# Performance work log

Measured on AMD Instinct MI355X. Metric: run time of the kernel, lower is better.

The kernel has to match this reference:

```python
import jax, jax.numpy as jnp
import numpy as np

KDIM = 16

def setup_inputs() -> dict:
    key = jax.random.key(0)
    k1, k2, k3, k4 = jax.random.split(key, 4)
    bs, k, din, dout, T = 512, 8, 1024, 1024, 8
    x = jax.random.normal(k1, (bs, k, din), dtype=jnp.float32)
    # template weights: list of (din, dout) params -> stacked (T, din, dout)
    w = 0.01 * jax.random.normal(k2, (T, din, dout), dtype=jnp.float32)
    # gll_read: GroupLinearLayer(din, kdim, 1) -> (1, din, kdim)
    w_read = 0.01 * jax.random.normal(k3, (1, din, KDIM), dtype=jnp.float32)
    # gll_write: GroupLinearLayer(dout, kdim, T) -> (T, dout, kdim)
    w_write = 0.01 * jax.random.normal(k4, (T, dout, KDIM), dtype=jnp.float32)
    return {"x": x, "w": w, "w_read": w_read, "w_write": w_write}

def reference(x, w, w_read, w_write):
    bs, k, din = x.shape
    dout = w.shape[-1]
    xf = x.reshape(bs * k, din)                       # (N, din)
    x_read = xf @ w_read[0]                           # (N, kdim)  query per token
    x_next = jnp.einsum('nd,tde->nte', xf, w)         # (N, T, dout) all template outputs
    x_write = jnp.einsum('nte,tek->ntk', x_next, w_write)  # (N, T, kdim) keys
    logits = jnp.einsum('nk,ntk->nt', x_read, x_write)     # (N, T)
    att = jax.nn.softmax(logits, axis=-1)                  # softmax over templates
    out = jnp.einsum('nt,nte->ne', att, x_next)            # weighted combine (mean over size-1 dim is identity)
    return out.reshape(bs, k, dout)
```

## Files before the change

kernel.cpp:

```cpp
#include <hip/hip_runtime.h>
#include <stdint.h>

typedef unsigned short u16;
typedef __attribute__((ext_vector_type(8))) short bf16x8;
typedef __attribute__((ext_vector_type(4))) float f32x4;
typedef __attribute__((ext_vector_type(4))) unsigned short u16x4;

#define AS1 __attribute__((address_space(1)))
#define AS3 __attribute__((address_space(3)))

static __device__ __forceinline__ u16 f2bf(float f) {
  union { float f; uint32_t u; } c; c.f = f;
  return (u16)((c.u + 0x7FFFu + ((c.u >> 16) & 1u)) >> 16);
}

__global__ __launch_bounds__(256) void k_prep(const float* __restrict__ x,
                                              u16* __restrict__ abf,
                                              const float* __restrict__ w,
                                              u16* __restrict__ bt,
                                              const float* __restrict__ ww,
                                              float* __restrict__ w2s) {
  __shared__ char smem[16896];
  const int bid = blockIdx.x;
  const int tid = threadIdx.x;

  if (bid < 256) {
    float (*wwT)[264] = (float(*)[264])smem;
    const int lane = tid & 63, wv = tid >> 6;
    const int t = (bid >> 3) & 7;
    const int d0 = (bid & 7) * 128 + wv * 32;
    const int ez4 = bid >> 6;
    const int ez = ez4 * 256;
    const int fr = lane & 15, koff = (lane >> 4) * 8;
    const float* wp = w + ((size_t)t << 20);
    const float* wwp = ww + (t << 14);
    for (int it = 0; it < 16; ++it) {
      int idx = it * 256 + tid;
      wwT[idx & 15][idx >> 4] = wwp[(size_t)(ez + (idx >> 4)) * 16 + (idx & 15)];
    }
    __syncthreads();
    f32x4 acc[2] = {};
    for (int kk = 0; kk < 256; kk += 32) {
      const int eL = kk + koff;
      float4 b0 = *(const float4*)&wwT[fr][eL];
      float4 b1 = *(const float4*)&wwT[fr][eL + 4];
      bf16x8 b;
      ((u16*)&b)[0] = f2bf(b0.x); ((u16*)&b)[1] = f2bf(b0.y);
      ((u16*)&b)[2] = f2bf(b0.z); ((u16*)&b)[3] = f2bf(b0.w);
      ((u16*)&b)[4] = f2bf(b1.x); ((u16*)&b)[5] = f2bf(b1.y);
      ((u16*)&b)[6] = f2bf(b1.z); ((u16*)&b)[7] = f2bf(b1.w);
#pragma unroll
      for (int m = 0; m < 2; ++m) {
        const float* ap = wp + (size_t)(d0 + m * 16 + fr) * 1024 + ez + eL;
        float4 a0 = *(const float4*)ap;
        float4 a1 = *(const float4*)(ap + 4);
        bf16x8 a;
        ((u16*)&a)[0] = f2bf(a0.x); ((u16*)&a)[1] = f2bf(a0.y);
        ((u16*)&a)[2] = f2bf(a0.z); ((u16*)&a)[3] = f2bf(a0.w);
        ((u16*)&a)[4] = f2bf(a1.x); ((u16*)&a)[5] = f2bf(a1.y);
        ((u16*)&a)[6] = f2bf(a1.z); ((u16*)&a)[7] = f2bf(a1.w);
        acc[m] = __builtin_amdgcn_mfma_f32_16x16x32_bf16(a, b, acc[m], 0, 0, 0);
      }
    }
    float* slot = w2s + ((size_t)ez4 << 17);
#pragma unroll
    for (int m = 0; m < 2; ++m)
#pragma unroll
      for (int i = 0; i < 4; ++i) {
        int d = d0 + m * 16 + ((lane >> 4) << 2) + i;
        slot[(((size_t)t << 10) + d) * 16 + fr] = acc[m][i];
      }
  } else if (bid < 4352) {
    int i = (bid - 256) * 256 + tid;
    float4 v = reinterpret_cast<const float4*>(x)[i];
    u16x4 o = { f2bf(v.x), f2bf(v.y), f2bf(v.z), f2bf(v.w) };
    reinterpret_cast<u16x4*>(abf)[i] = o;
  } else {
    u16 (*tile)[65] = (u16(*)[65])smem;
    const int tb = bid - 4352;
    const int t = tb >> 8, rem = tb & 255;
    const int e0 = (rem & 15) * 64, d0 = (rem >> 4) * 64;
    const int tx = tid & 63, ty = tid >> 6;
    const float* wp = w + ((size_t)t << 20);
    u16* bp = bt + ((size_t)t << 20);
    for (int rr = 0; rr < 16; ++rr) {
      int r = rr * 4 + ty;
      tile[r][tx] = f2bf(wp[(size_t)(d0 + r) * 1024 + (e0 + tx)]);
    }
    __syncthreads();
    for (int rr = 0; rr < 16; ++rr) {
      int r = rr * 4 + ty;
      bp[(size_t)(e0 + r) * 1024 + (d0 + tx)] = tile[tx][r];
    }
  }
}

__global__ __launch_bounds__(256) void k_bt2(const float* __restrict__ wread,
                                             const float* __restrict__ w2s,
                                             u16* __restrict__ bt2) {
  int i = blockIdx.x * 256 + threadIdx.x;
  int r = i >> 10, d = i & 1023;
  float v;
  if (r < 16) v = wread[d * 16 + r];
  else {
    int t = (r - 16) >> 4, k = (r - 16) & 15;
    size_t off = (((size_t)t << 10) + d) * 16 + k;
    v = w2s[off] + w2s[(1ull << 17) + off] + w2s[(2ull << 17) + off]
      + w2s[(3ull << 17) + off];
  }
  bt2[i] = f2bf(v);
}

__global__ __launch_bounds__(256) void k_p(const u16* __restrict__ abf,
                                           const u16* __restrict__ bt2,
                                           float* __restrict__ Ps) {
  const int tid = threadIdx.x, lane = tid & 63, wv = tid >> 6;
  const int row0 = blockIdx.x * 64 + wv * 16;
  const int k0 = blockIdx.y * 256;
  const int fr = lane & 15, koff = (lane >> 4) * 8;
  f32x4 acc[9] = {};
  for (int kk = 0; kk < 256; kk += 32) {
    bf16x8 a = *(const bf16x8*)&abf[(size_t)(row0 + fr) * 1024 + k0 + kk + koff];
#pragma unroll
    for (int n = 0; n < 9; ++n) {
      bf16x8 b = *(const bf16x8*)&bt2[(size_t)(n * 16 + fr) * 1024 + k0 + kk + koff];
      acc[n] = __builtin_amdgcn_mfma_f32_16x16x32_bf16(a, b, acc[n], 0, 0, 0);
    }
  }
  float* slot = Ps + (size_t)blockIdx.y * 589824;
  const int rbase = row0 + ((lane >> 4) << 2);
#pragma unroll
  for (int n = 0; n < 9; ++n)
#pragma unroll
    for (int i = 0; i < 4; ++i)
      slot[(size_t)(rbase + i) * 144 + n * 16 + fr] = acc[n][i];
}

__global__ __launch_bounds__(256) void k_soft(const float* __restrict__ Ps,
                                              float* __restrict__ att) {
  __shared__ float lg[32][8];
  const int rl = threadIdx.x >> 3, tt = threadIdx.x & 7;
  const int r = blockIdx.x * 32 + rl;
  const float* p = Ps + (size_t)r * 144;
  f32x4 x0 = {}, x1 = {}, x2 = {}, x3 = {};
  f32x4 y0 = {}, y1 = {}, y2 = {}, y3 = {};
#pragma unroll
  for (int z = 0; z < 4; ++z) {
    const float* pz = p + (size_t)z * 589824;
    x0 += *(const f32x4*)(pz);      x1 += *(const f32x4*)(pz + 4);
    x2 += *(const f32x4*)(pz + 8);  x3 += *(const f32x4*)(pz + 12);
    const float* qz = pz + 16 + tt * 16;
    y0 += *(const f32x4*)(qz);      y1 += *(const f32x4*)(qz + 4);
    y2 += *(const f32x4*)(qz + 8);  y3 += *(const f32x4*)(qz + 12);
  }
  float acc = x0[0]*y0[0] + x0[1]*y0[1] + x0[2]*y0[2] + x0[3]*y0[3]
            + x1[0]*y1[0] + x1[1]*y1[1] + x1[2]*y1[2] + x1[3]*y1[3]
            + x2[0]*y2[0] + x2[1]*y2[1] + x2[2]*y2[2] + x2[3]*y2[3]
            + x3[0]*y3[0] + x3[1]*y3[1] + x3[2]*y3[2] + x3[3]*y3[3];
  lg[rl][tt] = acc;
  __syncthreads();
  float m = lg[rl][0];
#pragma unroll
  for (int j = 1; j < 8; ++j) m = fmaxf(m, lg[rl][j]);
  float s = 0.f;
#pragma unroll
  for (int j = 0; j < 8; ++j) s += __expf(lg[rl][j] - m);
  att[(size_t)r * 8 + tt] = __expf(lg[rl][tt] - m) / s;
}

#define BAR()   asm volatile("s_barrier" ::: "memory")
#define LGKM0() asm volatile("s_waitcnt lgkmcnt(0)" ::: "memory")
#define VM6()   asm volatile("s_waitcnt vmcnt(6)" ::: "memory")
#define VM0()   asm volatile("s_waitcnt vmcnt(0)" ::: "memory")

template <int MODE>
__global__ __launch_bounds__(512, 2) void k_gemm256(const u16* __restrict__ abf,
                                                    const u16* __restrict__ bt,
                                                    const float* __restrict__ att,
                                                    float* __restrict__ out,
                                                    char* __restrict__ part) {
  __shared__ char lds[133120];
  float* lAtt = (float*)(lds + 131072);

  const int tid = threadIdx.x;
  const int lane = tid & 63;
  const int wv = tid >> 6;
  const int wr = wv >> 2, wc = wv & 3;

  int id = (blockIdx.z * gridDim.y + blockIdx.y) * gridDim.x + blockIdx.x;
  const int xcd = id & 7, pos = id >> 3;
  const int bz = xcd >> 1;
  const int by = (xcd & 1) * 8 + (pos & 7);
  const int bx = pos >> 3;
  const int bm = by * 256, bn = bx * 256, t0 = bz * 2;

  { int r = tid >> 1, c = tid & 1;
    lAtt[r * 2 + c] = att[(size_t)(bm + r) * 8 + t0 + c]; }

  const int l7 = lane & 7, lq = lane >> 4, l15 = lane & 15;
  const int srow = lane >> 3;
  const int scg = l7 ^ srow;
  const char* Abase = (const char*)abf;
  const char* Bbase = (const char*)bt;
  const size_t aSt0 = (size_t)(bm + wv * 16 + srow) * 2048 + scg * 16;
  const size_t bSt0 = (size_t)(bn + wv * 16 + srow) * 2048 + scg * 16;
  const int sDst = wv * 2048;
  const int aRd = (wr * 64 + l15) * 128;
  const int bRd = 32768 + (wc * 32 + l15) * 128;
  const int g0 = ((lq) ^ l7) * 16;
  const int g1 = ((4 + lq) ^ l7) * 16;

#define STAGE_A(bufo, h, tile) do {                                         \
    const char* s_ = Abase + aSt0 + (size_t)(h) * 262144 + ((tile) & 15) * 128; \
    __builtin_amdgcn_global_load_lds((const AS1 void*)s_,                   \
        (AS3 void*)(lds + (bufo) + (h) * 16384 + sDst), 16, 0, 0);          \
    __builtin_amdgcn_global_load_lds((const AS1 void*)(s_ + 16384),         \
        (AS3 void*)(lds + (bufo) + (h) * 16384 + sDst + 1024), 16, 0, 0);   \
  } while (0)
#define STAGE_B(bufo, g, tile) do {                                         \
    const char* s_ = Bbase + (size_t)(t0 + ((tile) >> 4)) * 2097152         \
                   + bSt0 + (size_t)(g) * 262144 + ((tile) & 15) * 128;     \
    __builtin_amdgcn_global_load_lds((const AS1 void*)s_,                   \
        (AS3 void*)(lds + (bufo) + 32768 + (g) * 16384 + sDst), 16, 0, 0);  \
    __builtin_amdgcn_global_load_lds((const AS1 void*)(s_ + 16384),         \
        (AS3 void*)(lds + (bufo) + 32768 + (g) * 16384 + sDst + 1024), 16, 0, 0); \
  } while (0)
#define LDA(bufo, h) do {                                                   \
    const char* p_ = lds + (bufo) + (h) * 16384 + aRd;                      \
    _Pragma("unroll") for (int mm = 0; mm < 4; ++mm) {                      \
      a[mm][0] = *(const bf16x8*)(p_ + mm * 2048 + g0);                     \
      a[mm][1] = *(const bf16x8*)(p_ + mm * 2048 + g1); }                   \
  } while (0)
#define LDB(bufo, g, br) do {                                               \
    const char* p_ = lds + (bufo) + (g) * 16384 + bRd;                      \
    _Pragma("unroll") for (int nn = 0; nn < 2; ++nn) {                      \
      br[nn][0] = *(const bf16x8*)(p_ + nn * 2048 + g0);                    \
      br[nn][1] = *(const bf16x8*)(p_ + nn * 2048 + g1); }                  \
  } while (0)
#define MFQ(h, g, br) do {                                                  \
    __builtin_amdgcn_s_setprio(1);                                          \
    _Pragma("unroll") for (int mm = 0; mm < 4; ++mm)                        \
    _Pragma("unroll") for (int nn = 0; nn < 2; ++nn) {                      \
      acc[(h)*4+mm][(g)*2+nn] = __builtin_amdgcn_mfma_f32_16x16x32_bf16(    \
          a[mm][0], br[nn][0], acc[(h)*4+mm][(g)*2+nn], 0, 0, 0);           \
      acc[(h)*4+mm][(g)*2+nn] = __builtin_amdgcn_mfma_f32_16x16x32_bf16(    \
          a[mm][1], br[nn][1], acc[(h)*4+mm][(g)*2+nn], 0, 0, 0); }         \
    __builtin_amdgcn_s_setprio(0);                                          \
  } while (0)

  f32x4 acc[8][4] = {};
  bf16x8 a[4][2], b0[2][2], b1[2][2];

  STAGE_A(0, 0, 0); STAGE_B(0, 0, 0); STAGE_B(0, 1, 0); STAGE_A(0, 1, 0);
  STAGE_A(65536, 0, 1); STAGE_B(65536, 0, 1); STAGE_B(65536, 1, 1);
  VM6(); BAR();

  for (int i = 0; i < 15; ++i) {
    if (i == 8) {
#pragma unroll
      for (int m = 0; m < 8; ++m) {
        const int h_ = m >> 2, mm_ = m & 3;
#pragma unroll
        for (int ii = 0; ii < 4; ++ii) {
          const int r_ = h_ * 128 + wr * 64 + mm_ * 16 + lq * 4 + ii;
          const float sc = lAtt[r_ * 2] / lAtt[r_ * 2 + 1];
#pragma unroll
          for (int n = 0; n < 4; ++n) acc[m][n][ii] *= sc;
        }
      }
    }
    const int j1 = 2 * i + 1, j2 = 2 * i + 2, j3 = 2 * i + 3;
    LDA(0, 0); LDB(0, 0, b0); STAGE_A(65536, 1, j1);
    BAR(); LGKM0(); MFQ(0, 0, b0); BAR();
    LDB(0, 1, b1); STAGE_A(0, 0, j2);
    BAR(); LGKM0(); MFQ(0, 1, b1); BAR();
    LDA(0, 1); STAGE_B(0, 0, j2);
    BAR(); LGKM0(); MFQ(1, 1, b1); BAR();
    STAGE_B(0, 1, j2);
    BAR(); MFQ(1, 0, b0); VM6(); BAR();
    LDA(65536, 0); LDB(65536, 0, b0); STAGE_A(0, 1, j2);
    BAR(); LGKM0(); MFQ(0, 0, b0); BAR();
    LDB(65536, 1, b1); STAGE_A(65536, 0, j3);
    BAR(); LGKM0(); MFQ(0, 1, b1); BAR();
    LDA(65536, 1); STAGE_B(65536, 0, j3);
    BAR(); LGKM0(); MFQ(1, 1, b1); BAR();
    STAGE_B(65536, 1, j3);
    BAR(); MFQ(1, 0, b0); VM6(); BAR();
  }
  LDA(0, 0); LDB(0, 0, b0); STAGE_A(65536, 1, 31);
  BAR(); LGKM0(); MFQ(0, 0, b0); BAR();
  LDB(0, 1, b1);
  BAR(); LGKM0(); MFQ(0, 1, b1); BAR();
  LDA(0, 1);
  BAR(); LGKM0(); MFQ(1, 1, b1); BAR();
  BAR(); MFQ(1, 0, b0); VM0(); BAR();
  LDA(65536, 0); LDB(65536, 0, b0);
  BAR(); LGKM0(); MFQ(0, 0, b0); BAR();
  LDB(65536, 1, b1);
  BAR(); LGKM0(); MFQ(0, 1, b1); BAR();
  LDA(65536, 1);
  BAR(); LGKM0(); MFQ(1, 1, b1); BAR();
  BAR(); MFQ(1, 0, b0); BAR();

#pragma unroll
  for (int m = 0; m < 8; ++m) {
    const int h_ = m >> 2, mm_ = m & 3;
#pragma unroll
    for (int ii = 0; ii < 4; ++ii) {
      const int rl = h_ * 128 + wr * 64 + mm_ * 16 + lq * 4 + ii;
      const float sc = lAtt[rl * 2 + 1];
      const int row = bm + rl;
#pragma unroll
      for (int n = 0; n < 4; ++n) {
        const int g_ = n >> 1, nn_ = n & 1;
        const int col = bn + g_ * 128 + wc * 32 + nn_ * 16 + l15;
        const float v = acc[m][n][ii] * sc;
        if (MODE == 0) {
          unsafeAtomicAdd(&out[(size_t)row * 1024 + col], v);
        } else {
          ((u16*)part)[((size_t)bz << 22) + (size_t)row * 1024 + col] = f2bf(v);
        }
      }
    }
  }
#undef STAGE_A
#undef STAGE_B
#undef LDA
#undef LDB
#undef MFQ
}

__global__ __launch_bounds__(256) void k_reduce(const char* __restrict__ part,
                                                float* __restrict__ out) {
  const size_t i = ((size_t)blockIdx.x * 256 + threadIdx.x) * 4;
  const u16* p = (const u16*)part;
  f32x4 s = {};
#pragma unroll
  for (int z = 0; z < 4; ++z) {
    u16x4 v = *(const u16x4*)(p + ((size_t)z << 22) + i);
#pragma unroll
    for (int j = 0; j < 4; ++j) {
      union { uint32_t u; float f; } c; c.u = ((uint32_t)v[j]) << 16;
      s[j] += c.f;
    }
  }
  *(f32x4*)(out + i) = s;
}

extern "C" void kernel_launch(void* const* d_in, const int* in_sizes, int n_in,
                              void* d_out, int out_size, void* d_ws, size_t ws_size,
                              hipStream_t stream) {
  (void)in_sizes; (void)n_in;
  const float* x      = (const float*)d_in[0];
  const float* w      = (const float*)d_in[1];
  const float* wread  = (const float*)d_in[2];
  const float* wwrite = (const float*)d_in[3];
  float* out = (float*)d_out;

  char* ws = (char*)d_ws;
  u16*   Abf = (u16*)ws;
  u16*   BT  = (u16*)(ws + (8ull << 20));
  u16*   BT2 = (u16*)(ws + (24ull << 20));
  float* Ps  = (float*)(ws + (25ull << 20));
  float* att = (float*)(ws + (34ull << 20));
  float* W2s = (float*)(ws + (34ull << 20) + (128ull << 10));
  char*  part = ws + (37ull << 20);

  k_prep<<<6400, 256, 0, stream>>>(x, Abf, w, BT, wwrite, W2s);
  k_bt2<<<576, 256, 0, stream>>>(wread, W2s, BT2);
  k_p<<<dim3(64, 4), 256, 0, stream>>>(Abf, BT2, Ps);
  k_soft<<<128, 256, 0, stream>>>(Ps, att);

  const size_t base = 37ull << 20;
  if (ws_size >= base + (4ull << 23)) {
    k_gemm256<2><<<dim3(4, 16, 4), 512, 0, stream>>>(Abf, BT, att, out, part);
    k_reduce<<<4096, 256, 0, stream>>>(part, out);
  } else {
    hipMemsetAsync(d_out, 0, (size_t)out_size * sizeof(float), stream);
    k_gemm256<0><<<dim3(4, 16, 4), 512, 0, stream>>>(Abf, BT, att, out, part);
  }
}
```

Measured before the change: 110.8 us.

## Fuse split-K reduction into GEMM via last-arriver tile counter

Drops the separate k_reduce kernel. Each split-K GEMM block writes its bf16 partials in a thread-owned packed layout using 64-bit stores, then increments a per-tile atomic counter. The last of the four blocks for a tile sums the partials and writes fp32 output. This saves a kernel launch and the extra full pass over memory, but adds atomic and fence overhead and a serialized reduce tail in the last-arriving block.

```diff
diff --git a/kernel.cpp b/kernel.cpp
--- a/kernel.cpp
+++ b/kernel.cpp
@@ -12,6 +12,9 @@
 static __device__ __forceinline__ u16 f2bf(float f) {
   union { float f; uint32_t u; } c; c.f = f;
   return (u16)((c.u + 0x7FFFu + ((c.u >> 16) & 1u)) >> 16);
+}
+static __device__ __forceinline__ float bfu2f(unsigned v) {
+  union { uint32_t u; float f; } c; c.u = (v & 0xFFFFu) << 16; return c.f;
 }
 
 __global__ __launch_bounds__(256) void k_prep(const float* __restrict__ x,
@@ -137,7 +140,9 @@
 }
 
 __global__ __launch_bounds__(256) void k_soft(const float* __restrict__ Ps,
-                                              float* __restrict__ att) {
+                                              float* __restrict__ att,
+                                              int* __restrict__ cnt) {
+  if (blockIdx.x == 0 && threadIdx.x < 64) cnt[threadIdx.x] = 0;
   __shared__ float lg[32][8];
   const int rl = threadIdx.x >> 3, tt = threadIdx.x & 7;
   const int r = blockIdx.x * 32 + rl;
@@ -178,7 +183,8 @@
                                                     const u16* __restrict__ bt,
                                                     const float* __restrict__ att,
                                                     float* __restrict__ out,
-                                                    char* __restrict__ part) {
+                                                    char* __restrict__ part,
+                                                    int* __restrict__ cnt) {
   __shared__ char lds[133120];
   float* lAtt = (float*)(lds + 131072);
 
@@ -302,23 +308,69 @@
   BAR(); LGKM0(); MFQ(1, 1, b1); BAR();
   BAR(); MFQ(1, 0, b0); BAR();
 
-#pragma unroll
-  for (int m = 0; m < 8; ++m) {
-    const int h_ = m >> 2, mm_ = m & 3;
-#pragma unroll
-    for (int ii = 0; ii < 4; ++ii) {
-      const int rl = h_ * 128 + wr * 64 + mm_ * 16 + lq * 4 + ii;
-      const float sc = lAtt[rl * 2 + 1];
-      const int row = bm + rl;
-#pragma unroll
-      for (int n = 0; n < 4; ++n) {
-        const int g_ = n >> 1, nn_ = n & 1;
-        const int col = bn + g_ * 128 + wc * 32 + nn_ * 16 + l15;
-        const float v = acc[m][n][ii] * sc;
-        if (MODE == 0) {
-          unsafeAtomicAdd(&out[(size_t)row * 1024 + col], v);
-        } else {
-          ((u16*)part)[((size_t)bz << 22) + (size_t)row * 1024 + col] = f2bf(v);
+  if (MODE == 0) {
+#pragma unroll
+    for (int m = 0; m < 8; ++m) {
+      const int h_ = m >> 2, mm_ = m & 3;
+#pragma unroll
+      for (int ii = 0; ii < 4; ++ii) {
+        const int rl = h_ * 128 + wr * 64 + mm_ * 16 + lq * 4 + ii;
+        const float sc = lAtt[rl * 2 + 1];
+        const int row = bm + rl;
+#pragma unroll
+        for (int n = 0; n < 4; ++n) {
+          const int g_ = n >> 1, nn_ = n & 1;
+          const int col = bn + g_ * 128 + wc * 32 + nn_ * 16 + l15;
+          unsafeAtomicAdd(&out[(size_t)row * 1024 + col], acc[m][n][ii] * sc);
+        }
+      }
+    }
+  } else {
+    const int tileid = by * 4 + bx;
+    unsigned long long* p64 = (unsigned long long*)part;
+    const size_t ownbase = (size_t)(tileid * 4 + bz) * 16384 + tid;
+#pragma unroll
+    for (int m = 0; m < 8; ++m) {
+      const int h_ = m >> 2, mm_ = m & 3;
+#pragma unroll
+      for (int ii = 0; ii < 4; ++ii) {
+        const int rl = h_ * 128 + wr * 64 + mm_ * 16 + lq * 4 + ii;
+        const float sc = lAtt[rl * 2 + 1];
+        unsigned long long pk = 0;
+#pragma unroll
+        for (int n = 0; n < 4; ++n)
+          pk |= (unsigned long long)f2bf(acc[m][n][ii] * sc) << (16 * n);
+        __hip_atomic_store(&p64[ownbase + (size_t)(m * 4 + ii) * 512], pk,
+                           __ATOMIC_RELAXED, __HIP_MEMORY_SCOPE_SYSTEM);
+      }
+    }
+    asm volatile("s_waitcnt vmcnt(0)" ::: "memory");
+    __syncthreads();
+    volatile int* flag = (volatile int*)lds;
+    if (tid == 0) {
+      int old = __hip_atomic_fetch_add(&cnt[tileid], 1, __ATOMIC_ACQ_REL,
+                                       __HIP_MEMORY_SCOPE_AGENT);
+      *flag = old;
+    }
+    __syncthreads();
+    if (*flag == 3) {
+      const size_t tb = (size_t)tileid * 4 * 16384 + tid;
+      for (int pair = 0; pair < 32; ++pair) {
+        float s[4] = {0.f, 0.f, 0.f, 0.f};
+#pragma unroll
+        for (int z = 0; z < 4; ++z) {
+          unsigned long long v = __hip_atomic_load(
+              &p64[tb + (size_t)z * 16384 + (size_t)pair * 512],
+              __ATOMIC_RELAXED, __HIP_MEMORY_SCOPE_SYSTEM);
+#pragma unroll
+          for (int n = 0; n < 4; ++n) s[n] += bfu2f((unsigned)(v >> (16 * n)));
+        }
+        const int m = pair >> 2, ii = pair & 3;
+        const int row = bm + (m >> 2) * 128 + wr * 64 + (m & 3) * 16 + lq * 4 + ii;
+#pragma unroll
+        for (int n = 0; n < 4; ++n) {
+          const int col = bn + (n >> 1) * 128 + wc * 32 + (n & 1) * 16 + l15;
+          out[(size_t)row * 1024 + col] = s[n];
         }
       }
     }
@@ -328,23 +380,6 @@
 #undef LDA
 #undef LDB
 #undef MFQ
-}
-
-__global__ __launch_bounds__(256) void k_reduce(const char* __restrict__ part,
-                                                float* __restrict__ out) {
-  const size_t i = ((size_t)blockIdx.x * 256 + threadIdx.x) * 4;
-  const u16* p = (const u16*)part;
-  f32x4 s = {};
-#pragma unroll
-  for (int z = 0; z < 4; ++z) {
-    u16x4 v = *(const u16x4*)(p + ((size_t)z << 22) + i);
-#pragma unroll
-    for (int j = 0; j < 4; ++j) {
-      union { uint32_t u; float f; } c; c.u = ((uint32_t)v[j]) << 16;
-      s[j] += c.f;
-    }
-  }
-  *(f32x4*)(out + i) = s;
 }
 
 extern "C" void kernel_launch(void* const* d_in, const int* in_sizes, int n_in,
@@ -361,6 +396,7 @@
   u16*   Abf = (u16*)ws;
   u16*   BT  = (u16*)(ws + (8ull << 20));
   u16*   BT2 = (u16*)(ws + (24ull << 20));
+  int*   cnt = (int*)(ws + (24ull << 20) + (512ull << 10));
   float* Ps  = (float*)(ws + (25ull << 20));
   float* att = (float*)(ws + (34ull << 20));
   float* W2s = (float*)(ws + (34ull << 20) + (128ull << 10));
@@ -369,14 +405,12 @@
   k_prep<<<6400, 256, 0, stream>>>(x, Abf, w, BT, wwrite, W2s);
   k_bt2<<<576, 256, 0, stream>>>(wread, W2s, BT2);
   k_p<<<dim3(64, 4), 256, 0, stream>>>(Abf, BT2, Ps);
-  k_soft<<<128, 256, 0, stream>>>(Ps, att);
-
-  const size_t base = 37ull << 20;
-  if (ws_size >= base + (4ull << 23)) {
-    k_gemm256<2><<<dim3(4, 16, 4), 512, 0, stream>>>(Abf, BT, att, out, part);
-    k_reduce<<<4096, 256, 0, stream>>>(part, out);
+  k_soft<<<128, 256, 0, stream>>>(Ps, att, cnt);
+
+  if (ws_size >= (37ull << 20) + (32ull << 20)) {
+    k_gemm256<2><<<dim3(4, 16, 4), 512, 0, stream>>>(Abf, BT, att, out, part, cnt);
   } else {
     hipMemsetAsync(d_out, 0, (size_t)out_size * sizeof(float), stream);
-    k_gemm256<0><<<dim3(4, 16, 4), 512, 0, stream>>>(Abf, BT, att, out, part);
-  }
-}
+    k_gemm256<0><<<dim3(4, 16, 4), 512, 0, stream>>>(Abf, BT, att, out, part, cnt);
+  }
+}
```

Measured after the change: 116.7 us. +5.3%, slower.

## Fuse W·Wwrite precompute into transpose blocks using the staged bf16 tile

Applied to the files above, without the earlier changes.

Removes the 256 separate MFMA blocks that re-read all of w to compute W·W_write. Each transpose block now loads its matching 64x16 slice of w_write and computes partial products from the bf16 tile already in shared memory, using scalar FMAs. It writes 16 e-slice partials, which k_bt2 then sums instead of 4. This saves one full read of w (32MB) at the cost of scalar FMA work and more partial-sum traffic, and the workspace layout moves accordingly.

```diff
diff --git a/kernel.cpp b/kernel.cpp
--- a/kernel.cpp
+++ b/kernel.cpp
@@ -12,6 +12,9 @@
 static __device__ __forceinline__ u16 f2bf(float f) {
   union { float f; uint32_t u; } c; c.f = f;
   return (u16)((c.u + 0x7FFFu + ((c.u >> 16) & 1u)) >> 16);
+}
+static __device__ __forceinline__ float bfu2f(unsigned v) {
+  union { uint32_t u; float f; } c; c.u = (v & 0xFFFFu) << 16; return c.f;
 }
 
 __global__ __launch_bounds__(256) void k_prep(const float* __restrict__ x,
@@ -20,64 +23,18 @@
                                               u16* __restrict__ bt,
                                               const float* __restrict__ ww,
                                               float* __restrict__ w2s) {
-  __shared__ char smem[16896];
   const int bid = blockIdx.x;
   const int tid = threadIdx.x;
 
-  if (bid < 256) {
-    float (*wwT)[264] = (float(*)[264])smem;
-    const int lane = tid & 63, wv = tid >> 6;
-    const int t = (bid >> 3) & 7;
-    const int d0 = (bid & 7) * 128 + wv * 32;
-    const int ez4 = bid >> 6;
-    const int ez = ez4 * 256;
-    const int fr = lane & 15, koff = (lane >> 4) * 8;
-    const float* wp = w + ((size_t)t << 20);
-    const float* wwp = ww + (t << 14);
-    for (int it = 0; it < 16; ++it) {
-      int idx = it * 256 + tid;
-      wwT[idx & 15][idx >> 4] = wwp[(size_t)(ez + (idx >> 4)) * 16 + (idx & 15)];
-    }
-    __syncthreads();
-    f32x4 acc[2] = {};
-    for (int kk = 0; kk < 256; kk += 32) {
-      const int eL = kk + koff;
-      float4 b0 = *(const float4*)&wwT[fr][eL];
-      float4 b1 = *(const float4*)&wwT[fr][eL + 4];
-      bf16x8 b;
-      ((u16*)&b)[0] = f2bf(b0.x); ((u16*)&b)[1] = f2bf(b0.y);
-      ((u16*)&b)[2] = f2bf(b0.z); ((u16*)&b)[3] = f2bf(b0.w);
-      ((u16*)&b)[4] = f2bf(b1.x); ((u16*)&b)[5] = f2bf(b1.y);
-      ((u16*)&b)[6] = f2bf(b1.z); ((u16*)&b)[7] = f2bf(b1.w);
-#pragma unroll
-      for (int m = 0; m < 2; ++m) {
-        const float* ap = wp + (size_t)(d0 + m * 16 + fr) * 1024 + ez + eL;
-        float4 a0 = *(const float4*)ap;
-        float4 a1 = *(const float4*)(ap + 4);
-        bf16x8 a;
-        ((u16*)&a)[0] = f2bf(a0.x); ((u16*)&a)[1] = f2bf(a0.y);
-        ((u16*)&a)[2] = f2bf(a0.z); ((u16*)&a)[3] = f2bf(a0.w);
-        ((u16*)&a)[4] = f2bf(a1.x); ((u16*)&a)[5] = f2bf(a1.y);
-        ((u16*)&a)[6] = f2bf(a1.z); ((u16*)&a)[7] = f2bf(a1.w);
-        acc[m] = __builtin_amdgcn_mfma_f32_16x16x32_bf16(a, b, acc[m], 0, 0, 0);
-      }
-    }
-    float* slot = w2s + ((size_t)ez4 << 17);
-#pragma unroll
-    for (int m = 0; m < 2; ++m)
-#pragma unroll
-      for (int i = 0; i < 4; ++i) {
-        int d = d0 + m * 16 + ((lane >> 4) << 2) + i;
-        slot[(((size_t)t << 10) + d) * 16 + fr] = acc[m][i];
-      }
-  } else if (bid < 4352) {
-    int i = (bid - 256) * 256 + tid;
+  if (bid < 4096) {
+    int i = bid * 256 + tid;
     float4 v = reinterpret_cast<const float4*>(x)[i];
     u16x4 o = { f2bf(v.x), f2bf(v.y), f2bf(v.z), f2bf(v.w) };
     reinterpret_cast<u16x4*>(abf)[i] = o;
   } else {
-    u16 (*tile)[65] = (u16(*)[65])smem;
-    const int tb = bid - 4352;
+    __shared__ u16 tile[64][65];
+    __shared__ float wwL[64][16];
+    const int tb = bid - 4096;
     const int t = tb >> 8, rem = tb & 255;
     const int e0 = (rem & 15) * 64, d0 = (rem >> 4) * 64;
     const int tx = tid & 63, ty = tid >> 6;
@@ -87,10 +44,26 @@
       int r = rr * 4 + ty;
       tile[r][tx] = f2bf(wp[(size_t)(d0 + r) * 1024 + (e0 + tx)]);
     }
+#pragma unroll
+    for (int p = 0; p < 4; ++p) {
+      int idx = p * 256 + tid;
+      wwL[idx >> 4][idx & 15] = ww[(t << 14) + (e0 + (idx >> 4)) * 16 + (idx & 15)];
+    }
     __syncthreads();
     for (int rr = 0; rr < 16; ++rr) {
       int r = rr * 4 + ty;
       bp[(size_t)(e0 + r) * 1024 + (d0 + tx)] = tile[tx][r];
+    }
+    float* slot = w2s + ((size_t)(rem & 15) << 17);
+#pragma unroll
+    for (int p = 0; p < 4; ++p) {
+      int id2 = p * 256 + tid;
+      int dl = id2 >> 4, k = id2 & 15;
+      float s = 0.f;
+#pragma unroll 8
+      for (int c = 0; c < 64; ++c)
+        s = fmaf(bfu2f(tile[dl][c]), wwL[c][k], s);
+      slot[(size_t)t * 16384 + d0 * 16 + id2] = s;
     }
   }
 }
@@ -105,8 +78,9 @@
   else {
     int t = (r - 16) >> 4, k = (r - 16) & 15;
     size_t off = (((size_t)t << 10) + d) * 16 + k;
-    v = w2s[off] + w2s[(1ull << 17) + off] + w2s[(2ull << 17) + off]
-      + w2s[(3ull << 17) + off];
+    v = 0.f;
+#pragma unroll
+    for (int esl = 0; esl < 16; ++esl) v += w2s[((size_t)esl << 17) + off];
   }
   bt2[i] = f2bf(v);
 }
@@ -363,16 +337,15 @@
   u16*   BT2 = (u16*)(ws + (24ull << 20));
   float* Ps  = (float*)(ws + (25ull << 20));
   float* att = (float*)(ws + (34ull << 20));
-  float* W2s = (float*)(ws + (34ull << 20) + (128ull << 10));
-  char*  part = ws + (37ull << 20);
-
-  k_prep<<<6400, 256, 0, stream>>>(x, Abf, w, BT, wwrite, W2s);
+  float* W2s = (float*)(ws + (35ull << 20));
+  char*  part = ws + (43ull << 20);
+
+  k_prep<<<6144, 256, 0, stream>>>(x, Abf, w, BT, wwrite, W2s);
   k_bt2<<<576, 256, 0, stream>>>(wread, W2s, BT2);
   k_p<<<dim3(64, 4), 256, 0, stream>>>(Abf, BT2, Ps);
   k_soft<<<128, 256, 0, stream>>>(Ps, att);
 
-  const size_t base = 37ull << 20;
-  if (ws_size >= base + (4ull << 23)) {
+  if (ws_size >= (43ull << 20) + (32ull << 20)) {
     k_gemm256<2><<<dim3(4, 16, 4), 512, 0, stream>>>(Abf, BT, att, out, part);
     k_reduce<<<4096, 256, 0, stream>>>(part, out);
   } else {
```

After: 141.4 us. 27.7% more time.

## Replace split-T 256x256 GEMM with full-K 128x128 tile, drop reduction pass

Applied to the files above, without the earlier changes.

The main GEMM moves from 256x256 tiles split over four template pairs (with bf16 partials and a separate reduce kernel) to 128x128 tiles that each loop over all eight templates (K=8192). Each tile writes fp32 output directly. Online softmax rescaling is applied at every template boundary. This removes the partial-buffer write/read traffic and one kernel launch, and avoids bf16 rounding of partials. In exchange it gives lower per-tile data reuse, more global loads per FLOP, and a simpler double-buffered pipeline with 256 blocks.

```diff
diff --git a/kernel.cpp b/kernel.cpp
--- a/kernel.cpp
+++ b/kernel.cpp
@@ -170,32 +170,28 @@
 
 #define BAR()   asm volatile("s_barrier" ::: "memory")
 #define LGKM0() asm volatile("s_waitcnt lgkmcnt(0)" ::: "memory")
-#define VM6()   asm volatile("s_waitcnt vmcnt(6)" ::: "memory")
-#define VM0()   asm volatile("s_waitcnt vmcnt(0)" ::: "memory")
-
-template <int MODE>
-__global__ __launch_bounds__(512, 2) void k_gemm256(const u16* __restrict__ abf,
+#define VM4()   asm volatile("s_waitcnt vmcnt(4)" ::: "memory")
+
+__global__ __launch_bounds__(512, 2) void k_gemm128(const u16* __restrict__ abf,
                                                     const u16* __restrict__ bt,
                                                     const float* __restrict__ att,
-                                                    float* __restrict__ out,
-                                                    char* __restrict__ part) {
-  __shared__ char lds[133120];
-  float* lAtt = (float*)(lds + 131072);
+                                                    float* __restrict__ out) {
+  __shared__ char lds[69632];
+  float* lAtt = (float*)(lds + 65536);
 
   const int tid = threadIdx.x;
   const int lane = tid & 63;
   const int wv = tid >> 6;
   const int wr = wv >> 2, wc = wv & 3;
 
-  int id = (blockIdx.z * gridDim.y + blockIdx.y) * gridDim.x + blockIdx.x;
+  int id = blockIdx.y * gridDim.x + blockIdx.x;
   const int xcd = id & 7, pos = id >> 3;
-  const int bz = xcd >> 1;
-  const int by = (xcd & 1) * 8 + (pos & 7);
-  const int bx = pos >> 3;
-  const int bm = by * 256, bn = bx * 256, t0 = bz * 2;
-
-  { int r = tid >> 1, c = tid & 1;
-    lAtt[r * 2 + c] = att[(size_t)(bm + r) * 8 + t0 + c]; }
+  const int bx = pos & 7;
+  const int by = xcd * 4 + (pos >> 3);
+  const int bm = by * 128, bn = bx * 128;
+
+  { int idx = tid * 2; int r = idx >> 3, c = idx & 7;
+    *(float2*)&lAtt[idx] = *(const float2*)&att[(size_t)(bm + r) * 8 + c]; }
 
   const int l7 = lane & 7, lq = lane >> 4, l15 = lane & 15;
   const int srow = lane >> 3;
@@ -206,151 +202,96 @@
   const size_t bSt0 = (size_t)(bn + wv * 16 + srow) * 2048 + scg * 16;
   const int sDst = wv * 2048;
   const int aRd = (wr * 64 + l15) * 128;
-  const int bRd = 32768 + (wc * 32 + l15) * 128;
-  const int g0 = ((lq) ^ l7) * 16;
+  const int bRd = 16384 + (wc * 32 + l15) * 128;
+  const int g0 = (lq ^ l7) * 16;
   const int g1 = ((4 + lq) ^ l7) * 16;
 
-#define STAGE_A(bufo, h, tile) do {                                         \
-    const char* s_ = Abase + aSt0 + (size_t)(h) * 262144 + ((tile) & 15) * 128; \
+#define STAGE_A(bufo, js_) do {                                             \
+    int js = (js_); if (js > 127) js = 127;                                 \
+    const char* s_ = Abase + aSt0 + (js & 15) * 128;                        \
     __builtin_amdgcn_global_load_lds((const AS1 void*)s_,                   \
-        (AS3 void*)(lds + (bufo) + (h) * 16384 + sDst), 16, 0, 0);          \
+        (AS3 void*)(lds + (bufo) + sDst), 16, 0, 0);                        \
     __builtin_amdgcn_global_load_lds((const AS1 void*)(s_ + 16384),         \
-        (AS3 void*)(lds + (bufo) + (h) * 16384 + sDst + 1024), 16, 0, 0);   \
+        (AS3 void*)(lds + (bufo) + sDst + 1024), 16, 0, 0);                 \
   } while (0)
-#define STAGE_B(bufo, g, tile) do {                                         \
-    const char* s_ = Bbase + (size_t)(t0 + ((tile) >> 4)) * 2097152         \
-                   + bSt0 + (size_t)(g) * 262144 + ((tile) & 15) * 128;     \
+#define STAGE_B(bufo, js_) do {                                             \
+    int js = (js_); if (js > 127) js = 127;                                 \
+    const char* s_ = Bbase + (size_t)(js >> 4) * 2097152                    \
+                   + bSt0 + (js & 15) * 128;                                \
     __builtin_amdgcn_global_load_lds((const AS1 void*)s_,                   \
-        (AS3 void*)(lds + (bufo) + 32768 + (g) * 16384 + sDst), 16, 0, 0);  \
+        (AS3 void*)(lds + (bufo) + 16384 + sDst), 16, 0, 0);                \
     __builtin_amdgcn_global_load_lds((const AS1 void*)(s_ + 16384),         \
-        (AS3 void*)(lds + (bufo) + 32768 + (g) * 16384 + sDst + 1024), 16, 0, 0); \
+        (AS3 void*)(lds + (bufo) + 16384 + sDst + 1024), 16, 0, 0);         \
   } while (0)
-#define LDA(bufo, h) do {                                                   \
-    const char* p_ = lds + (bufo) + (h) * 16384 + aRd;                      \
-    _Pragma("unroll") for (int mm = 0; mm < 4; ++mm) {                      \
-      a[mm][0] = *(const bf16x8*)(p_ + mm * 2048 + g0);                     \
-      a[mm][1] = *(const bf16x8*)(p_ + mm * 2048 + g1); }                   \
+#define LDAB(bufo) do {                                                     \
+    const char* pa = lds + (bufo) + aRd;                                    \
+    _Pragma("unroll") for (int m = 0; m < 4; ++m) {                         \
+      a[m][0] = *(const bf16x8*)(pa + m * 2048 + g0);                       \
+      a[m][1] = *(const bf16x8*)(pa + m * 2048 + g1); }                     \
+    const char* pb = lds + (bufo) + bRd;                                    \
+    _Pragma("unroll") for (int n = 0; n < 2; ++n) {                         \
+      b[n][0] = *(const bf16x8*)(pb + n * 2048 + g0);                       \
+      b[n][1] = *(const bf16x8*)(pb + n * 2048 + g1); }                     \
   } while (0)
-#define LDB(bufo, g, br) do {                                               \
-    const char* p_ = lds + (bufo) + (g) * 16384 + bRd;                      \
-    _Pragma("unroll") for (int nn = 0; nn < 2; ++nn) {                      \
-      br[nn][0] = *(const bf16x8*)(p_ + nn * 2048 + g0);                    \
-      br[nn][1] = *(const bf16x8*)(p_ + nn * 2048 + g1); }                  \
-  } while (0)
-#define MFQ(h, g, br) do {                                                  \
+#define MFQ(ks) do {                                                        \
     __builtin_amdgcn_s_setprio(1);                                          \
-    _Pragma("unroll") for (int mm = 0; mm < 4; ++mm)                        \
-    _Pragma("unroll") for (int nn = 0; nn < 2; ++nn) {                      \
-      acc[(h)*4+mm][(g)*2+nn] = __builtin_amdgcn_mfma_f32_16x16x32_bf16(    \
-          a[mm][0], br[nn][0], acc[(h)*4+mm][(g)*2+nn], 0, 0, 0);           \
-      acc[(h)*4+mm][(g)*2+nn] = __builtin_amdgcn_mfma_f32_16x16x32_bf16(    \
-          a[mm][1], br[nn][1], acc[(h)*4+mm][(g)*2+nn], 0, 0, 0); }         \
+    _Pragma("unroll") for (int m = 0; m < 4; ++m)                           \
+    _Pragma("unroll") for (int n = 0; n < 2; ++n)                           \
+      acc[m][n] = __builtin_amdgcn_mfma_f32_16x16x32_bf16(                  \
+          a[m][ks], b[n][ks], acc[m][n], 0, 0, 0);                          \
     __builtin_amdgcn_s_setprio(0);                                          \
   } while (0)
 
-  f32x4 acc[8][4] = {};
-  bf16x8 a[4][2], b0[2][2], b1[2][2];
-
-  STAGE_A(0, 0, 0); STAGE_B(0, 0, 0); STAGE_B(0, 1, 0); STAGE_A(0, 1, 0);
-  STAGE_A(65536, 0, 1); STAGE_B(65536, 0, 1); STAGE_B(65536, 1, 1);
-  VM6(); BAR();
-
-  for (int i = 0; i < 15; ++i) {
-    if (i == 8) {
-#pragma unroll
-      for (int m = 0; m < 8; ++m) {
-        const int h_ = m >> 2, mm_ = m & 3;
+  f32x4 acc[4][2] = {};
+  bf16x8 a[4][2], b[2][2];
+
+  STAGE_A(0, 0); STAGE_B(0, 0); STAGE_A(32768, 1); STAGE_B(32768, 1);
+  VM4(); BAR();
+
+  for (int j = 0; j < 128; ++j) {
+    const int bufc = (j & 1) * 32768;
+    if (j && !(j & 15)) {
+      const int t = j >> 4;
+#pragma unroll
+      for (int m = 0; m < 4; ++m)
 #pragma unroll
         for (int ii = 0; ii < 4; ++ii) {
-          const int r_ = h_ * 128 + wr * 64 + mm_ * 16 + lq * 4 + ii;
-          const float sc = lAtt[r_ * 2] / lAtt[r_ * 2 + 1];
-#pragma unroll
-          for (int n = 0; n < 4; ++n) acc[m][n][ii] *= sc;
+          const int rl = wr * 64 + m * 16 + lq * 4 + ii;
+          const float sc = lAtt[rl * 8 + t - 1] / lAtt[rl * 8 + t];
+#pragma unroll
+          for (int n = 0; n < 2; ++n) acc[m][n][ii] *= sc;
         }
+    }
+    LDAB(bufc);
+    LGKM0(); MFQ(0); BAR();
+    STAGE_A(bufc, j + 2); STAGE_B(bufc, j + 2);
+    MFQ(1);
+    VM4(); BAR();
+  }
+
+#pragma unroll
+  for (int m = 0; m < 4; ++m)
+#pragma unroll
+    for (int ii = 0; ii < 4; ++ii) {
+      const int rl = wr * 64 + m * 16 + lq * 4 + ii;
+      const float sc = lAtt[rl * 8 + 7];
+      const int row = bm + rl;
+#pragma unroll
+      for (int n = 0; n < 2; ++n) {
+        const int col = bn + wc * 32 + n * 16 + l15;
+        out[(size_t)row * 1024 + col] = acc[m][n][ii] * sc;
       }
     }
-    const int j1 = 2 * i + 1, j2 = 2 * i + 2, j3 = 2 * i + 3;
-    LDA(0, 0); LDB(0, 0, b0); STAGE_A(65536, 1, j1);
-    BAR(); LGKM0(); MFQ(0, 0, b0); BAR();
-    LDB(0, 1, b1); STAGE_A(0, 0, j2);
-    BAR(); LGKM0(); MFQ(0, 1, b1); BAR();
-    LDA(0, 1); STAGE_B(0, 0, j2);
-    BAR(); LGKM0(); MFQ(1, 1, b1); BAR();
-    STAGE_B(0, 1, j2);
-    BAR(); MFQ(1, 0, b0); VM6(); BAR();
-    LDA(65536, 0); LDB(65536, 0, b0); STAGE_A(0, 1, j2);
-    BAR(); LGKM0(); MFQ(0, 0, b0); BAR();
-    LDB(65536, 1, b1); STAGE_A(65536, 0, j3);
-    BAR(); LGKM0(); MFQ(0, 1, b1); BAR();
-    LDA(65536, 1); STAGE_B(65536, 0, j3);
-    BAR(); LGKM0(); MFQ(1, 1, b1); BAR();
-    STAGE_B(65536, 1, j3);
-    BAR(); MFQ(1, 0, b0); VM6(); BAR();
-  }
-  LDA(0, 0); LDB(0, 0, b0); STAGE_A(65536, 1, 31);
-  BAR(); LGKM0(); MFQ(0, 0, b0); BAR();
-  LDB(0, 1, b1);
-  BAR(); LGKM0(); MFQ(0, 1, b1); BAR();
-  LDA(0, 1);
-  BAR(); LGKM0(); MFQ(1, 1, b1); BAR();
-  BAR(); MFQ(1, 0, b0); VM0(); BAR();
-  LDA(65536, 0); LDB(65536, 0, b0);
-  BAR(); LGKM0(); MFQ(0, 0, b0); BAR();
-  LDB(65536, 1, b1);
-  BAR(); LGKM0(); MFQ(0, 1, b1); BAR();
-  LDA(65536, 1);
-  BAR(); LGKM0(); MFQ(1, 1, b1); BAR();
-  BAR(); MFQ(1, 0, b0); BAR();
-
-#pragma unroll
-  for (int m = 0; m < 8; ++m) {
-    const int h_ = m >> 2, mm_ = m & 3;
-#pragma unroll
-    for (int ii = 0; ii < 4; ++ii) {
-      const int rl = h_ * 128 + wr * 64 + mm_ * 16 + lq * 4 + ii;
-      const float sc = lAtt[rl * 2 + 1];
-      const int row = bm + rl;
-#pragma unroll
-      for (int n = 0; n < 4; ++n) {
-        const int g_ = n >> 1, nn_ = n & 1;
-        const int col = bn + g_ * 128 + wc * 32 + nn_ * 16 + l15;
-        const float v = acc[m][n][ii] * sc;
-        if (MODE == 0) {
-          unsafeAtomicAdd(&out[(size_t)row * 1024 + col], v);
-        } else {
-          ((u16*)part)[((size_t)bz << 22) + (size_t)row * 1024 + col] = f2bf(v);
-        }
-      }
-    }
-  }
 #undef STAGE_A
 #undef STAGE_B
-#undef LDA
-#undef LDB
+#undef LDAB
 #undef MFQ
-}
-
-__global__ __launch_bounds__(256) void k_reduce(const char* __restrict__ part,
-                                                float* __restrict__ out) {
-  const size_t i = ((size_t)blockIdx.x * 256 + threadIdx.x) * 4;
-  const u16* p = (const u16*)part;
-  f32x4 s = {};
-#pragma unroll
-  for (int z = 0; z < 4; ++z) {
-    u16x4 v = *(const u16x4*)(p + ((size_t)z << 22) + i);
-#pragma unroll
-    for (int j = 0; j < 4; ++j) {
-      union { uint32_t u; float f; } c; c.u = ((uint32_t)v[j]) << 16;
-      s[j] += c.f;
-    }
-  }
-  *(f32x4*)(out + i) = s;
 }
 
 extern "C" void kernel_launch(void* const* d_in, const int* in_sizes, int n_in,
                               void* d_out, int out_size, void* d_ws, size_t ws_size,
                               hipStream_t stream) {
-  (void)in_sizes; (void)n_in;
+  (void)in_sizes; (void)n_in; (void)out_size; (void)ws_size;
   const float* x      = (const float*)d_in[0];
   const float* w      = (const float*)d_in[1];
   const float* wread  = (const float*)d_in[2];
@@ -364,19 +305,10 @@
   float* Ps  = (float*)(ws + (25ull << 20));
   float* att = (float*)(ws + (34ull << 20));
   float* W2s = (float*)(ws + (34ull << 20) + (128ull << 10));
-  char*  part = ws + (37ull << 20);
 
   k_prep<<<6400, 256, 0, stream>>>(x, Abf, w, BT, wwrite, W2s);
   k_bt2<<<576, 256, 0, stream>>>(wread, W2s, BT2);
   k_p<<<dim3(64, 4), 256, 0, stream>>>(Abf, BT2, Ps);
   k_soft<<<128, 256, 0, stream>>>(Ps, att);
-
-  const size_t base = 37ull << 20;
-  if (ws_size >= base + (4ull << 23)) {
-    k_gemm256<2><<<dim3(4, 16, 4), 512, 0, stream>>>(Abf, BT, att, out, part);
-    k_reduce<<<4096, 256, 0, stream>>>(part, out);
-  } else {
-    hipMemsetAsync(d_out, 0, (size_t)out_size * sizeof(float), stream);
-    k_gemm256<0><<<dim3(4, 16, 4), 512, 0, stream>>>(Abf, BT, att, out, part);
-  }
-}
+  k_gemm128<<<dim3(8, 32), 512, 0, stream>>>(Abf, BT, att, out);
+}
```

New measurement: 121.5 us. 9.7% more time.
